# Kernel tuning notes

Hardware: AMD Instinct MI355X
Metric: run time of the kernel (lower is better)

## Reference

```python
import jax, jax.numpy as jnp
import numpy as np

N, E, H, PIN, PEIN, POUT, L = 50000, 800000, 128, 16, 8, 8, 4
EPS = 1e-7


def setup_inputs() -> dict:
    key = jax.random.key(0)
    ks = jax.random.split(key, 24)
    f = jax.random.normal
    inp = {
        'x': f(ks[0], (N, PIN), jnp.float32),
        'edge_attr': f(ks[1], (E, PEIN), jnp.float32),
        'edge_index': jax.random.randint(ks[2], (2, E), 0, N, jnp.int32),
        # encoders
        'node_W': f(ks[3], (PIN, H)) * (1.0 / np.sqrt(PIN)),
        'node_b': jnp.zeros((H,)),
        'edge_W': f(ks[4], (PEIN, H)) * (1.0 / np.sqrt(PEIN)),
        'edge_b': jnp.zeros((H,)),
        # GENConv params per layer (stacked over L): MLP Linear(H,2H)->LN->ReLU->Linear(2H,H), temp t
        'W1': f(ks[5], (L, H, 2 * H)) * (1.0 / np.sqrt(H)),
        'b1': jnp.zeros((L, 2 * H)),
        'g1': jnp.ones((L, 2 * H)),
        'be1': jnp.zeros((L, 2 * H)),
        'W2': f(ks[6], (L, 2 * H, H)) * (1.0 / np.sqrt(2 * H)),
        'b2': jnp.zeros((L, H)),
        't': jnp.ones((L,)),
        # DeepGCNLayer LayerNorms
        'ng': jnp.ones((L, H)),
        'nb': jnp.zeros((L, H)),
        # output head
        'out_W': f(ks[7], (H, POUT)) * (1.0 / np.sqrt(H)),
        'out_b': jnp.zeros((POUT,)),
    }
    return inp


def _layernorm(x, g, b):
    mu = jnp.mean(x, -1, keepdims=True)
    v = jnp.mean(jnp.square(x - mu), -1, keepdims=True)
    return (x - mu) * jax.lax.rsqrt(v + 1e-5) * g + b


def reference(x, edge_attr, edge_index, node_W, node_b, edge_W, edge_b,
              W1, b1, g1, be1, W2, b2, t, ng, nb, out_W, out_b):
    src, dst = edge_index[0], edge_index[1]

    def genconv(h, e, i):
        # message: relu(x_j + edge_attr) + eps   [E, H]
        msg = jax.nn.relu(h[src] + e) + EPS
        # softmax aggregation over edges per destination node, temperature t[i]
        s = msg * t[i]
        m = jax.ops.segment_max(s, dst, num_segments=N)  # [N, H]
        w = jnp.exp(s - m[dst])
        denom = jax.ops.segment_sum(w, dst, num_segments=N)
        agg = jax.ops.segment_sum(msg * w, dst, num_segments=N)
        agg = jnp.where(denom > 0, agg / jnp.maximum(denom, EPS), 0.0)
        # root add, then 2-layer MLP (Linear -> LN -> ReLU -> Linear)
        z = agg + h
        z = jax.nn.relu(_layernorm(z @ W1[i] + b1[i], g1[i], be1[i]))
        return z @ W2[i] + b2[i]

    h = x @ node_W + node_b                      # node encoder
    e = jax.nn.sigmoid(edge_attr @ edge_W + edge_b)  # edge encoder
    h = genconv(h, e, 0)                         # layers[0].conv only
    for i in range(1, L):                        # res+ blocks
        z = jax.nn.relu(_layernorm(h, ng[i], nb[i]))
        h = h + genconv(z, e, i)
    h = jax.nn.relu(_layernorm(h, ng[0], nb[0]))  # layers[0] norm+act; dropout=eval identity
    return h @ out_W + out_b
```

## Files before the change

kernel.cpp:

```cpp
#include <hip/hip_runtime.h>
#include <hip/hip_bf16.h>

#define NN 50000
#define NE 800000
#define HH 128
#define PIN_ 16
#define PEIN_ 8
#define POUT_ 8
#define LAYERS_ 4
#define EPSM 1e-7f

typedef __bf16 bf16x8 __attribute__((ext_vector_type(8)));
typedef float f32x4 __attribute__((ext_vector_type(4)));

union BF8 { bf16x8 v; unsigned short s[8]; };

__device__ inline unsigned short f2bf(float f) {
  unsigned int u = __float_as_uint(f);
  u += 0x7FFFu + ((u >> 16) & 1u);
  return (unsigned short)(u >> 16);
}


__global__ void count_deg_kernel(const int* __restrict__ dst, int* __restrict__ deg) {
  int i = blockIdx.x * blockDim.x + threadIdx.x;
  if (i < NE) atomicAdd(&deg[dst[i]], 1);
}

__global__ __launch_bounds__(1024) void scan_kernel(const int* __restrict__ deg,
                                                    int* __restrict__ row_ptr,
                                                    int* __restrict__ cursor, int n) {
  __shared__ int wsum[16];
  __shared__ int carry_s;
  int t = threadIdx.x;
  int lane = t & 63, wv = t >> 6;
  if (t == 0) carry_s = 0;
  __syncthreads();
  for (int base = 0; base < n; base += 1024) {
    int i = base + t;
    int v = (i < n) ? deg[i] : 0;
    int x = v;
#pragma unroll
    for (int off = 1; off < 64; off <<= 1) {
      int y = __shfl_up(x, off, 64);
      if (lane >= off) x += y;
    }
    if (lane == 63) wsum[wv] = x;
    __syncthreads();
    if (wv == 0 && lane < 16) {
      int s = wsum[lane];
#pragma unroll
      for (int off = 1; off < 16; off <<= 1) {
        int y = __shfl_up(s, off, 16);
        if (lane >= off) s += y;
      }
      wsum[lane] = s;
    }
    __syncthreads();
    int waveExcl = (wv > 0) ? wsum[wv - 1] : 0;
    int carry = carry_s;
    int excl = carry + waveExcl + x - v;
    if (i < n) { row_ptr[i] = excl; cursor[i] = excl; }
    __syncthreads();
    if (t == 1023) carry_s = carry + wsum[15];
    __syncthreads();
  }
  if (t == 0) row_ptr[n] = carry_s;
}

__global__ void scatter_kernel(const int* __restrict__ src, const int* __restrict__ dst,
                               int* __restrict__ cursor, int2* __restrict__ csr) {
  int i = blockIdx.x * blockDim.x + threadIdx.x;
  if (i < NE) {
    int d = dst[i];
    int pos = atomicAdd(&cursor[d], 1);
    csr[pos] = make_int2(src[i], i);
  }
}


__global__ __launch_bounds__(256) void prep_weights_kernel(
    const float* __restrict__ W1, const float* __restrict__ W2,
    unsigned short* __restrict__ W1T, unsigned short* __restrict__ W2T) {
  int idx = blockIdx.x * 256 + threadIdx.x;
  if (idx >= LAYERS_ * 256 * 128) return;
  int l = idx >> 15, r = idx & 32767;
  int n = r >> 7, k = r & 127;
  W1T[idx] = f2bf(W1[(l << 15) + k * 256 + n]);
  int c = r >> 8, kk = r & 255;
  W2T[idx] = f2bf(W2[(l << 15) + kk * 128 + c]);
}


__global__ __launch_bounds__(128) void node_enc_kernel(const float* __restrict__ x,
                                                       const float* __restrict__ W,
                                                       const float* __restrict__ b,
                                                       float* __restrict__ h) {
  __shared__ float xs[16 * PIN_];
  int f = threadIdx.x;
  float w[PIN_];
#pragma unroll
  for (int k = 0; k < PIN_; ++k) w[k] = W[k * HH + f];
  float bf = b[f];
  int base = blockIdx.x * 16;
  xs[f] = x[(size_t)base * PIN_ + f];
  xs[f + 128] = x[(size_t)base * PIN_ + f + 128];
  __syncthreads();
#pragma unroll
  for (int r = 0; r < 16; ++r) {
    float acc = bf;
#pragma unroll
    for (int k = 0; k < PIN_; ++k) acc = fmaf(xs[r * PIN_ + k], w[k], acc);
    h[(size_t)(base + r) * HH + f] = acc;
  }
}


__global__ __launch_bounds__(256) void aggregate_kernel(
    const int* __restrict__ row_ptr, const int2* __restrict__ csr,
    const float* __restrict__ edge_attr, const float* __restrict__ edge_W,
    const float* __restrict__ edge_b, const float* __restrict__ z,
    const float* __restrict__ t_all, int layer, float* __restrict__ u) {
  int wv = threadIdx.x >> 6, lane = threadIdx.x & 63;
  int n = blockIdx.x * 4 + wv;
  if (n >= NN) return;
  float ew0[PEIN_], ew1[PEIN_];
#pragma unroll
  for (int k = 0; k < PEIN_; ++k) {
    ew0[k] = edge_W[k * HH + lane];
    ew1[k] = edge_W[k * HH + lane + 64];
  }
  float eb0 = edge_b[lane], eb1 = edge_b[lane + 64];
  float t = t_all[layer];
  int beg = row_ptr[n], end = row_ptr[n + 1];
  float m0 = -1e30f, m1 = -1e30f, d0 = 0.f, d1 = 0.f, a0 = 0.f, a1 = 0.f;
  for (int p = beg; p < end; ++p) {
    int2 se = csr[p];
    const float4* ea = (const float4*)(edge_attr + (size_t)se.y * PEIN_);
    float4 A = ea[0], B = ea[1];
    float acc0 = eb0, acc1 = eb1;
    acc0 = fmaf(A.x, ew0[0], acc0); acc0 = fmaf(A.y, ew0[1], acc0);
    acc0 = fmaf(A.z, ew0[2], acc0); acc0 = fmaf(A.w, ew0[3], acc0);
    acc0 = fmaf(B.x, ew0[4], acc0); acc0 = fmaf(B.y, ew0[5], acc0);
    acc0 = fmaf(B.z, ew0[6], acc0); acc0 = fmaf(B.w, ew0[7], acc0);
    acc1 = fmaf(A.x, ew1[0], acc1); acc1 = fmaf(A.y, ew1[1], acc1);
    acc1 = fmaf(A.z, ew1[2], acc1); acc1 = fmaf(A.w, ew1[3], acc1);
    acc1 = fmaf(B.x, ew1[4], acc1); acc1 = fmaf(B.y, ew1[5], acc1);
    acc1 = fmaf(B.z, ew1[6], acc1); acc1 = fmaf(B.w, ew1[7], acc1);
    float e0 = __builtin_amdgcn_rcpf(1.f + __expf(-acc0));
    float e1 = __builtin_amdgcn_rcpf(1.f + __expf(-acc1));
    const float* zr = z + (size_t)se.x * HH;
    float zj0 = zr[lane], zj1 = zr[lane + 64];
    float msg0 = fmaxf(zj0 + e0, 0.f) + EPSM;
    float msg1 = fmaxf(zj1 + e1, 0.f) + EPSM;
    float s0 = msg0 * t, s1 = msg1 * t;
    float nm0 = fmaxf(m0, s0), nm1 = fmaxf(m1, s1);
    float sc0 = __expf(m0 - nm0), sc1 = __expf(m1 - nm1);
    float w0 = __expf(s0 - nm0), w1 = __expf(s1 - nm1);
    d0 = fmaf(d0, sc0, w0); d1 = fmaf(d1, sc1, w1);
    a0 = fmaf(a0, sc0, msg0 * w0); a1 = fmaf(a1, sc1, msg1 * w1);
    m0 = nm0; m1 = nm1;
  }
  float agg0 = (d0 > 0.f) ? a0 / fmaxf(d0, EPSM) : 0.f;
  float agg1 = (d1 > 0.f) ? a1 / fmaxf(d1, EPSM) : 0.f;
  const size_t ro = (size_t)n * HH;
  u[ro + lane] = agg0 + z[ro + lane];
  u[ro + lane + 64] = agg1 + z[ro + lane + 64];
}


__device__ inline int tswz(int r, int c) { return r * 256 + (c ^ ((r & 7) << 3)); }

__global__ __launch_bounds__(256) void mlp_fused_kernel(
    const float* __restrict__ uin,
    const unsigned short* __restrict__ W1T,
    const float* __restrict__ b1v, const float* __restrict__ g1v,
    const float* __restrict__ be1v,
    const unsigned short* __restrict__ W2T,
    const float* __restrict__ b2v,
    const float* __restrict__ res,
    const float* __restrict__ ngv, const float* __restrict__ nbv,
    float* __restrict__ hout, float* __restrict__ zout) {
  __shared__ __align__(16) unsigned short Tlds[4 * 16 * 256];
  int wv = threadIdx.x >> 6, lane = threadIdx.x & 63;
  int gw = blockIdx.x * 4 + wv;
  if (gw >= NN / 16) return;
  int row0 = gw * 16;
  int l15 = lane & 15, qg = lane >> 4;
  unsigned short* tl = Tlds + wv * 4096;

  BF8 afr[4];
#pragma unroll
  for (int kb = 0; kb < 4; ++kb) {
    const float* up = uin + (size_t)(row0 + l15) * HH + kb * 32 + qg * 8;
    float4 f0 = *(const float4*)up;
    float4 f1 = *(const float4*)(up + 4);
    afr[kb].s[0] = f2bf(f0.x); afr[kb].s[1] = f2bf(f0.y);
    afr[kb].s[2] = f2bf(f0.z); afr[kb].s[3] = f2bf(f0.w);
    afr[kb].s[4] = f2bf(f1.x); afr[kb].s[5] = f2bf(f1.y);
    afr[kb].s[6] = f2bf(f1.z); afr[kb].s[7] = f2bf(f1.w);
  }
  f32x4 acc1[16];
#pragma unroll
  for (int nb = 0; nb < 16; ++nb) acc1[nb] = (f32x4){0.f, 0.f, 0.f, 0.f};
#pragma unroll
  for (int nb = 0; nb < 16; ++nb) {
#pragma unroll
    for (int kb = 0; kb < 4; ++kb) {
      bf16x8 b = *(const bf16x8*)(W1T + (size_t)(nb * 16 + l15) * HH + kb * 32 + qg * 8);
      acc1[nb] = __builtin_amdgcn_mfma_f32_16x16x32_bf16(afr[kb].v, b, acc1[nb], 0, 0, 0);
    }
  }

  float sum1[4] = {0.f, 0.f, 0.f, 0.f};
#pragma unroll
  for (int nb = 0; nb < 16; ++nb) {
    float bb = b1v[nb * 16 + l15];
#pragma unroll
    for (int i = 0; i < 4; ++i) { acc1[nb][i] += bb; sum1[i] += acc1[nb][i]; }
  }
#pragma unroll
  for (int i = 0; i < 4; ++i) {
#pragma unroll
    for (int m = 1; m < 16; m <<= 1) sum1[i] += __shfl_xor(sum1[i], m, 64);
  }
  float mu1[4], sq1[4] = {0.f, 0.f, 0.f, 0.f};
#pragma unroll
  for (int i = 0; i < 4; ++i) mu1[i] = sum1[i] * (1.f / 256.f);
#pragma unroll
  for (int nb = 0; nb < 16; ++nb)
#pragma unroll
    for (int i = 0; i < 4; ++i) {
      float d = acc1[nb][i] - mu1[i];
      sq1[i] = fmaf(d, d, sq1[i]);
    }
#pragma unroll
  for (int i = 0; i < 4; ++i) {
#pragma unroll
    for (int m = 1; m < 16; m <<= 1) sq1[i] += __shfl_xor(sq1[i], m, 64);
  }
  float rstd1[4];
#pragma unroll
  for (int i = 0; i < 4; ++i) rstd1[i] = rsqrtf(sq1[i] * (1.f / 256.f) + 1e-5f);
#pragma unroll
  for (int nb = 0; nb < 16; ++nb) {
    int c = nb * 16 + l15;
    float g = g1v[c], be = be1v[c];
#pragma unroll
    for (int i = 0; i < 4; ++i) {
      float tv = fmaxf(fmaf((acc1[nb][i] - mu1[i]) * rstd1[i], g, be), 0.f);
      tl[tswz(4 * qg + i, c)] = f2bf(tv);
    }
  }

  f32x4 acc2[8];
#pragma unroll
  for (int nc = 0; nc < 8; ++nc) acc2[nc] = (f32x4){0.f, 0.f, 0.f, 0.f};
#pragma unroll
  for (int kb = 0; kb < 8; ++kb) {
    bf16x8 a2 = *(const bf16x8*)&tl[tswz(l15, kb * 32 + qg * 8)];
#pragma unroll
    for (int nc = 0; nc < 8; ++nc) {
      bf16x8 b = *(const bf16x8*)(W2T + (size_t)(nc * 16 + l15) * 256 + kb * 32 + qg * 8);
      acc2[nc] = __builtin_amdgcn_mfma_f32_16x16x32_bf16(a2, b, acc2[nc], 0, 0, 0);
    }
  }

  float sum2[4] = {0.f, 0.f, 0.f, 0.f};
#pragma unroll
  for (int nc = 0; nc < 8; ++nc) {
    int c = nc * 16 + l15;
    float bb = b2v[c];
#pragma unroll
    for (int i = 0; i < 4; ++i) {
      float v = acc2[nc][i] + bb;
      if (res) v += res[(size_t)(row0 + 4 * qg + i) * HH + c];
      acc2[nc][i] = v;
      sum2[i] += v;
    }
  }
#pragma unroll
  for (int nc = 0; nc < 8; ++nc) {
    int c = nc * 16 + l15;
#pragma unroll
    for (int i = 0; i < 4; ++i)
      hout[(size_t)(row0 + 4 * qg + i) * HH + c] = acc2[nc][i];
  }
#pragma unroll
  for (int i = 0; i < 4; ++i) {
#pragma unroll
    for (int m = 1; m < 16; m <<= 1) sum2[i] += __shfl_xor(sum2[i], m, 64);
  }
  float mu2[4], sq2[4] = {0.f, 0.f, 0.f, 0.f};
#pragma unroll
  for (int i = 0; i < 4; ++i) mu2[i] = sum2[i] * (1.f / 128.f);
#pragma unroll
  for (int nc = 0; nc < 8; ++nc)
#pragma unroll
    for (int i = 0; i < 4; ++i) {
      float d = acc2[nc][i] - mu2[i];
      sq2[i] = fmaf(d, d, sq2[i]);
    }
#pragma unroll
  for (int i = 0; i < 4; ++i) {
#pragma unroll
    for (int m = 1; m < 16; m <<= 1) sq2[i] += __shfl_xor(sq2[i], m, 64);
  }
  float rstd2[4];
#pragma unroll
  for (int i = 0; i < 4; ++i) rstd2[i] = rsqrtf(sq2[i] * (1.f / 128.f) + 1e-5f);
#pragma unroll
  for (int nc = 0; nc < 8; ++nc) {
    int c = nc * 16 + l15;
    float g = ngv[c], be = nbv[c];
#pragma unroll
    for (int i = 0; i < 4; ++i) {
      float zv = fmaxf(fmaf((acc2[nc][i] - mu2[i]) * rstd2[i], g, be), 0.f);
      zout[(size_t)(row0 + 4 * qg + i) * HH + c] = zv;
    }
  }
}


__global__ __launch_bounds__(256) void out_head_kernel(const float* __restrict__ zf,
                                                       const float* __restrict__ W,
                                                       const float* __restrict__ b,
                                                       float* __restrict__ out) {
  __shared__ float Wl[HH * POUT_];
  int t = threadIdx.x;
  for (int i = t; i < HH * POUT_; i += 256) Wl[i] = W[i];
  __syncthreads();
  int n = blockIdx.x * 32 + (t >> 3);
  int p = t & 7;
  if (n >= NN) return;
  float acc = b[p];
  const float* zr = zf + (size_t)n * HH;
#pragma unroll 8
  for (int k = 0; k < HH; ++k) acc = fmaf(zr[k], Wl[k * POUT_ + p], acc);
  out[(size_t)n * POUT_ + p] = acc;
}


extern "C" void kernel_launch(void* const* d_in, const int* in_sizes, int n_in,
                              void* d_out, int out_size, void* d_ws, size_t ws_size,
                              hipStream_t stream) {
  const float* x = (const float*)d_in[0];
  const float* edge_attr = (const float*)d_in[1];
  const int* edge_index = (const int*)d_in[2];
  const float* node_W = (const float*)d_in[3];
  const float* node_b = (const float*)d_in[4];
  const float* edge_W = (const float*)d_in[5];
  const float* edge_b = (const float*)d_in[6];
  const float* W1 = (const float*)d_in[7];
  const float* b1 = (const float*)d_in[8];
  const float* g1 = (const float*)d_in[9];
  const float* be1 = (const float*)d_in[10];
  const float* W2 = (const float*)d_in[11];
  const float* b2 = (const float*)d_in[12];
  const float* t_all = (const float*)d_in[13];
  const float* ng = (const float*)d_in[14];
  const float* nb = (const float*)d_in[15];
  const float* out_W = (const float*)d_in[16];
  const float* out_b = (const float*)d_in[17];

  const int* src = edge_index;
  const int* dst = edge_index + NE;

  char* w = (char*)d_ws;
  float* h = (float*)w;
  float* u = (float*)(w + 25600000);
  float* z = (float*)(w + 51200000);
  int* deg = (int*)(w + 76800000);
  int* row_ptr = (int*)(w + 76800000 + 204800);
  int* cursor = (int*)(w + 76800000 + 409600);
  int2* csr = (int2*)(w + 76800000 + 614400);
  unsigned short* W1Tb = (unsigned short*)(w + 83814400);
  unsigned short* W2Tb = (unsigned short*)(w + 83814400 + 262144);

  hipMemsetAsync(deg, 0, NN * sizeof(int), stream);
  count_deg_kernel<<<(NE + 255) / 256, 256, 0, stream>>>(dst, deg);
  scan_kernel<<<1, 1024, 0, stream>>>(deg, row_ptr, cursor, NN);
  scatter_kernel<<<(NE + 255) / 256, 256, 0, stream>>>(src, dst, cursor, csr);
  prep_weights_kernel<<<512, 256, 0, stream>>>(W1, W2, W1Tb, W2Tb);
  node_enc_kernel<<<NN / 16, 128, 0, stream>>>(x, node_W, node_b, h);

  const int mlp_blocks = (NN / 16 + 3) / 4;
  for (int i = 0; i < LAYERS_; ++i) {
    const float* zsrc = (i == 0) ? h : z;
    aggregate_kernel<<<NN / 4, 256, 0, stream>>>(row_ptr, csr, edge_attr, edge_W, edge_b,
                                                 zsrc, t_all, i, u);
    int zn = (i + 1) % LAYERS_;
    mlp_fused_kernel<<<mlp_blocks, 256, 0, stream>>>(
        u, W1Tb + (size_t)i * 32768, b1 + i * 256, g1 + i * 256, be1 + i * 256,
        W2Tb + (size_t)i * 32768, b2 + i * HH,
        (i == 0) ? nullptr : h,
        ng + zn * HH, nb + zn * HH, h, z);
  }
  out_head_kernel<<<(NN + 31) / 32, 256, 0, stream>>>(z, out_W, out_b, (float*)d_out);
}
```

Baseline: 1.116 ms.

## Store node features as packed bf16 and drop online max in softmax aggregation

Node activations z and aggregated u are now stored as interleaved packed bf16 pairs, which halves the bytes gathered per edge in the aggregation kernel and the bytes the MLP reads. The softmax aggregation loses its running-max rescaling and accumulates exp(msg*t) directly, removing two exps per element. This relies on msg*t staying small enough not to overflow, and it loses some precision. The MLP swaps MFMA operand order so each lane holds four consecutive columns, which allows float4 bias, gamma and output accesses and cuts the shuffle reductions to two steps. The fp32 z is written only in the last layer for the output head.

```diff
diff --git a/kernel.cpp b/kernel.cpp
--- a/kernel.cpp
+++ b/kernel.cpp
@@ -13,13 +13,16 @@
 typedef __bf16 bf16x8 __attribute__((ext_vector_type(8)));
 typedef float f32x4 __attribute__((ext_vector_type(4)));
 
-union BF8 { bf16x8 v; unsigned short s[8]; };
-
 __device__ inline unsigned short f2bf(float f) {
   unsigned int u = __float_as_uint(f);
   u += 0x7FFFu + ((u >> 16) & 1u);
   return (unsigned short)(u >> 16);
 }
+__device__ inline unsigned int packbf(float lo, float hi) {
+  return (unsigned int)f2bf(lo) | ((unsigned int)f2bf(hi) << 16);
+}
+__device__ inline float bflo(unsigned int p) { return __uint_as_float(p << 16); }
+__device__ inline float bfhi(unsigned int p) { return __uint_as_float(p & 0xFFFF0000u); }
 
 
 __global__ void count_deg_kernel(const int* __restrict__ dst, int* __restrict__ deg) {
@@ -81,37 +84,47 @@
 
 __global__ __launch_bounds__(256) void prep_weights_kernel(
     const float* __restrict__ W1, const float* __restrict__ W2,
-    unsigned short* __restrict__ W1T, unsigned short* __restrict__ W2T) {
+    unsigned short* __restrict__ W1Tp, unsigned short* __restrict__ W2T) {
   int idx = blockIdx.x * 256 + threadIdx.x;
   if (idx >= LAYERS_ * 256 * 128) return;
   int l = idx >> 15, r = idx & 32767;
-  int n = r >> 7, k = r & 127;
-  W1T[idx] = f2bf(W1[(l << 15) + k * 256 + n]);
+  int n = r >> 7, p = r & 127;
+  int k = (p >> 1) + ((p & 1) << 6);
+  W1Tp[idx] = f2bf(W1[(l << 15) + k * 256 + n]);
   int c = r >> 8, kk = r & 255;
   W2T[idx] = f2bf(W2[(l << 15) + kk * 128 + c]);
 }
 
 
-__global__ __launch_bounds__(128) void node_enc_kernel(const float* __restrict__ x,
-                                                       const float* __restrict__ W,
-                                                       const float* __restrict__ b,
-                                                       float* __restrict__ h) {
-  __shared__ float xs[16 * PIN_];
+__global__ __launch_bounds__(64) void node_enc_kernel(const float* __restrict__ x,
+                                                      const float* __restrict__ W,
+                                                      const float* __restrict__ b,
+                                                      float* __restrict__ h,
+                                                      unsigned int* __restrict__ hbp) {
+  __shared__ float xs[8 * PIN_];
   int f = threadIdx.x;
-  float w[PIN_];
-#pragma unroll
-  for (int k = 0; k < PIN_; ++k) w[k] = W[k * HH + f];
-  float bf = b[f];
-  int base = blockIdx.x * 16;
+  float w0[PIN_], w1[PIN_];
+#pragma unroll
+  for (int k = 0; k < PIN_; ++k) {
+    w0[k] = W[k * HH + f];
+    w1[k] = W[k * HH + f + 64];
+  }
+  float b0 = b[f], b1c = b[f + 64];
+  int base = blockIdx.x * 8;
   xs[f] = x[(size_t)base * PIN_ + f];
-  xs[f + 128] = x[(size_t)base * PIN_ + f + 128];
+  xs[f + 64] = x[(size_t)base * PIN_ + f + 64];
   __syncthreads();
 #pragma unroll
-  for (int r = 0; r < 16; ++r) {
-    float acc = bf;
-#pragma unroll
-    for (int k = 0; k < PIN_; ++k) acc = fmaf(xs[r * PIN_ + k], w[k], acc);
-    h[(size_t)(base + r) * HH + f] = acc;
+  for (int r = 0; r < 8; ++r) {
+    float a0 = b0, a1 = b1c;
+#pragma unroll
+    for (int k = 0; k < PIN_; ++k) {
+      a0 = fmaf(xs[r * PIN_ + k], w0[k], a0);
+      a1 = fmaf(xs[r * PIN_ + k], w1[k], a1);
+    }
+    h[(size_t)(base + r) * HH + f] = a0;
+    h[(size_t)(base + r) * HH + f + 64] = a1;
+    hbp[(size_t)(base + r) * 64 + f] = packbf(a0, a1);
   }
 }
 
@@ -119,8 +132,8 @@
 __global__ __launch_bounds__(256) void aggregate_kernel(
     const int* __restrict__ row_ptr, const int2* __restrict__ csr,
     const float* __restrict__ edge_attr, const float* __restrict__ edge_W,
-    const float* __restrict__ edge_b, const float* __restrict__ z,
-    const float* __restrict__ t_all, int layer, float* __restrict__ u) {
+    const float* __restrict__ edge_b, const unsigned int* __restrict__ zpk,
+    const float* __restrict__ t_all, int layer, unsigned int* __restrict__ upk) {
   int wv = threadIdx.x >> 6, lane = threadIdx.x & 63;
   int n = blockIdx.x * 4 + wv;
   if (n >= NN) return;
@@ -133,7 +146,8 @@
   float eb0 = edge_b[lane], eb1 = edge_b[lane + 64];
   float t = t_all[layer];
   int beg = row_ptr[n], end = row_ptr[n + 1];
-  float m0 = -1e30f, m1 = -1e30f, d0 = 0.f, d1 = 0.f, a0 = 0.f, a1 = 0.f;
+  unsigned int zs = zpk[(size_t)n * 64 + lane];
+  float d0 = 0.f, d1 = 0.f, a0 = 0.f, a1 = 0.f;
   for (int p = beg; p < end; ++p) {
     int2 se = csr[p];
     const float4* ea = (const float4*)(edge_attr + (size_t)se.y * PEIN_);
@@ -149,57 +163,47 @@
     acc1 = fmaf(B.z, ew1[6], acc1); acc1 = fmaf(B.w, ew1[7], acc1);
     float e0 = __builtin_amdgcn_rcpf(1.f + __expf(-acc0));
     float e1 = __builtin_amdgcn_rcpf(1.f + __expf(-acc1));
-    const float* zr = z + (size_t)se.x * HH;
-    float zj0 = zr[lane], zj1 = zr[lane + 64];
-    float msg0 = fmaxf(zj0 + e0, 0.f) + EPSM;
-    float msg1 = fmaxf(zj1 + e1, 0.f) + EPSM;
-    float s0 = msg0 * t, s1 = msg1 * t;
-    float nm0 = fmaxf(m0, s0), nm1 = fmaxf(m1, s1);
-    float sc0 = __expf(m0 - nm0), sc1 = __expf(m1 - nm1);
-    float w0 = __expf(s0 - nm0), w1 = __expf(s1 - nm1);
-    d0 = fmaf(d0, sc0, w0); d1 = fmaf(d1, sc1, w1);
-    a0 = fmaf(a0, sc0, msg0 * w0); a1 = fmaf(a1, sc1, msg1 * w1);
-    m0 = nm0; m1 = nm1;
+    unsigned int zp = zpk[(size_t)se.x * 64 + lane];
+    float msg0 = fmaxf(bflo(zp) + e0, 0.f) + EPSM;
+    float msg1 = fmaxf(bfhi(zp) + e1, 0.f) + EPSM;
+    float w0 = __expf(msg0 * t), w1 = __expf(msg1 * t);
+    d0 += w0; d1 += w1;
+    a0 = fmaf(msg0, w0, a0); a1 = fmaf(msg1, w1, a1);
   }
   float agg0 = (d0 > 0.f) ? a0 / fmaxf(d0, EPSM) : 0.f;
   float agg1 = (d1 > 0.f) ? a1 / fmaxf(d1, EPSM) : 0.f;
-  const size_t ro = (size_t)n * HH;
-  u[ro + lane] = agg0 + z[ro + lane];
-  u[ro + lane + 64] = agg1 + z[ro + lane + 64];
-}
-
-
-__device__ inline int tswz(int r, int c) { return r * 256 + (c ^ ((r & 7) << 3)); }
+  float u0 = agg0 + bflo(zs);
+  float u1 = agg1 + bfhi(zs);
+  upk[(size_t)n * 64 + lane] = packbf(u0, u1);
+}
+
 
 __global__ __launch_bounds__(256) void mlp_fused_kernel(
-    const float* __restrict__ uin,
-    const unsigned short* __restrict__ W1T,
+    const unsigned int* __restrict__ upk,
+    const unsigned short* __restrict__ W1Tp,
     const float* __restrict__ b1v, const float* __restrict__ g1v,
     const float* __restrict__ be1v,
     const unsigned short* __restrict__ W2T,
     const float* __restrict__ b2v,
     const float* __restrict__ res,
     const float* __restrict__ ngv, const float* __restrict__ nbv,
-    float* __restrict__ hout, float* __restrict__ zout) {
-  __shared__ __align__(16) unsigned short Tlds[4 * 16 * 256];
+    float* __restrict__ hout, float* __restrict__ zoutf,
+    unsigned int* __restrict__ zbp) {
+  __shared__ __align__(16) unsigned short Tlds[4 * 4096];
   int wv = threadIdx.x >> 6, lane = threadIdx.x & 63;
   int gw = blockIdx.x * 4 + wv;
   if (gw >= NN / 16) return;
   int row0 = gw * 16;
   int l15 = lane & 15, qg = lane >> 4;
+  int co = 4 * qg;
+  int sx = (l15 & 7) << 3;
   unsigned short* tl = Tlds + wv * 4096;
 
-  BF8 afr[4];
-#pragma unroll
-  for (int kb = 0; kb < 4; ++kb) {
-    const float* up = uin + (size_t)(row0 + l15) * HH + kb * 32 + qg * 8;
-    float4 f0 = *(const float4*)up;
-    float4 f1 = *(const float4*)(up + 4);
-    afr[kb].s[0] = f2bf(f0.x); afr[kb].s[1] = f2bf(f0.y);
-    afr[kb].s[2] = f2bf(f0.z); afr[kb].s[3] = f2bf(f0.w);
-    afr[kb].s[4] = f2bf(f1.x); afr[kb].s[5] = f2bf(f1.y);
-    afr[kb].s[6] = f2bf(f1.z); afr[kb].s[7] = f2bf(f1.w);
-  }
+  const unsigned short* ub =
+      (const unsigned short*)upk + (size_t)(row0 + l15) * HH + qg * 8;
+  bf16x8 ufr[4];
+#pragma unroll
+  for (int kb = 0; kb < 4; ++kb) ufr[kb] = *(const bf16x8*)(ub + kb * 32);
   f32x4 acc1[16];
 #pragma unroll
   for (int nb = 0; nb < 16; ++nb) acc1[nb] = (f32x4){0.f, 0.f, 0.f, 0.f};
@@ -207,117 +211,110 @@
   for (int nb = 0; nb < 16; ++nb) {
 #pragma unroll
     for (int kb = 0; kb < 4; ++kb) {
-      bf16x8 b = *(const bf16x8*)(W1T + (size_t)(nb * 16 + l15) * HH + kb * 32 + qg * 8);
-      acc1[nb] = __builtin_amdgcn_mfma_f32_16x16x32_bf16(afr[kb].v, b, acc1[nb], 0, 0, 0);
-    }
-  }
-
-  float sum1[4] = {0.f, 0.f, 0.f, 0.f};
+      bf16x8 wf = *(const bf16x8*)(W1Tp + (size_t)(nb * 16 + l15) * HH + kb * 32 + qg * 8);
+      acc1[nb] = __builtin_amdgcn_mfma_f32_16x16x32_bf16(wf, ufr[kb], acc1[nb], 0, 0, 0);
+    }
+  }
+
+  float sum1 = 0.f;
 #pragma unroll
   for (int nb = 0; nb < 16; ++nb) {
-    float bb = b1v[nb * 16 + l15];
-#pragma unroll
-    for (int i = 0; i < 4; ++i) { acc1[nb][i] += bb; sum1[i] += acc1[nb][i]; }
-  }
-#pragma unroll
-  for (int i = 0; i < 4; ++i) {
-#pragma unroll
-    for (int m = 1; m < 16; m <<= 1) sum1[i] += __shfl_xor(sum1[i], m, 64);
-  }
-  float mu1[4], sq1[4] = {0.f, 0.f, 0.f, 0.f};
-#pragma unroll
-  for (int i = 0; i < 4; ++i) mu1[i] = sum1[i] * (1.f / 256.f);
+    float4 bq = *(const float4*)(b1v + nb * 16 + co);
+    acc1[nb][0] += bq.x; acc1[nb][1] += bq.y;
+    acc1[nb][2] += bq.z; acc1[nb][3] += bq.w;
+    sum1 += acc1[nb][0] + acc1[nb][1] + acc1[nb][2] + acc1[nb][3];
+  }
+  sum1 += __shfl_xor(sum1, 16, 64);
+  sum1 += __shfl_xor(sum1, 32, 64);
+  float mu1 = sum1 * (1.f / 256.f);
+  float sq1 = 0.f;
 #pragma unroll
   for (int nb = 0; nb < 16; ++nb)
 #pragma unroll
     for (int i = 0; i < 4; ++i) {
-      float d = acc1[nb][i] - mu1[i];
-      sq1[i] = fmaf(d, d, sq1[i]);
-    }
-#pragma unroll
-  for (int i = 0; i < 4; ++i) {
-#pragma unroll
-    for (int m = 1; m < 16; m <<= 1) sq1[i] += __shfl_xor(sq1[i], m, 64);
-  }
-  float rstd1[4];
-#pragma unroll
-  for (int i = 0; i < 4; ++i) rstd1[i] = rsqrtf(sq1[i] * (1.f / 256.f) + 1e-5f);
+      float d = acc1[nb][i] - mu1;
+      sq1 = fmaf(d, d, sq1);
+    }
+  sq1 += __shfl_xor(sq1, 16, 64);
+  sq1 += __shfl_xor(sq1, 32, 64);
+  float rstd1 = rsqrtf(sq1 * (1.f / 256.f) + 1e-5f);
 #pragma unroll
   for (int nb = 0; nb < 16; ++nb) {
-    int c = nb * 16 + l15;
-    float g = g1v[c], be = be1v[c];
+    float4 gq = *(const float4*)(g1v + nb * 16 + co);
+    float4 eq = *(const float4*)(be1v + nb * 16 + co);
+    float t0 = fmaxf(fmaf((acc1[nb][0] - mu1) * rstd1, gq.x, eq.x), 0.f);
+    float t1 = fmaxf(fmaf((acc1[nb][1] - mu1) * rstd1, gq.y, eq.y), 0.f);
+    float t2 = fmaxf(fmaf((acc1[nb][2] - mu1) * rstd1, gq.z, eq.z), 0.f);
+    float t3 = fmaxf(fmaf((acc1[nb][3] - mu1) * rstd1, gq.w, eq.w), 0.f);
+    int ad = l15 * 256 + ((nb * 16 + co) ^ sx);
+    *(uint2*)(tl + ad) = make_uint2(packbf(t0, t1), packbf(t2, t3));
+  }
+
+  f32x4 acc2[8];
+#pragma unroll
+  for (int nc = 0; nc < 8; ++nc) acc2[nc] = (f32x4){0.f, 0.f, 0.f, 0.f};
+#pragma unroll
+  for (int kb = 0; kb < 8; ++kb) {
+    bf16x8 tf = *(const bf16x8*)(tl + l15 * 256 + ((kb * 32 + qg * 8) ^ sx));
+#pragma unroll
+    for (int nc = 0; nc < 8; ++nc) {
+      bf16x8 wf = *(const bf16x8*)(W2T + (size_t)(nc * 16 + l15) * 256 + kb * 32 + qg * 8);
+      acc2[nc] = __builtin_amdgcn_mfma_f32_16x16x32_bf16(wf, tf, acc2[nc], 0, 0, 0);
+    }
+  }
+
+  size_t rb = (size_t)(row0 + l15) * HH;
+  float sum2 = 0.f;
+#pragma unroll
+  for (int nc = 0; nc < 8; ++nc) {
+    float4 bq = *(const float4*)(b2v + nc * 16 + co);
+    acc2[nc][0] += bq.x; acc2[nc][1] += bq.y;
+    acc2[nc][2] += bq.z; acc2[nc][3] += bq.w;
+    if (res) {
+      float4 rq = *(const float4*)(res + rb + nc * 16 + co);
+      acc2[nc][0] += rq.x; acc2[nc][1] += rq.y;
+      acc2[nc][2] += rq.z; acc2[nc][3] += rq.w;
+    }
+    *(float4*)(hout + rb + nc * 16 + co) =
+        make_float4(acc2[nc][0], acc2[nc][1], acc2[nc][2], acc2[nc][3]);
+    sum2 += acc2[nc][0] + acc2[nc][1] + acc2[nc][2] + acc2[nc][3];
+  }
+  sum2 += __shfl_xor(sum2, 16, 64);
+  sum2 += __shfl_xor(sum2, 32, 64);
+  float mu2 = sum2 * (1.f / 128.f);
+  float sq2 = 0.f;
+#pragma unroll
+  for (int nc = 0; nc < 8; ++nc)
 #pragma unroll
     for (int i = 0; i < 4; ++i) {
-      float tv = fmaxf(fmaf((acc1[nb][i] - mu1[i]) * rstd1[i], g, be), 0.f);
-      tl[tswz(4 * qg + i, c)] = f2bf(tv);
-    }
-  }
-
-  f32x4 acc2[8];
-#pragma unroll
-  for (int nc = 0; nc < 8; ++nc) acc2[nc] = (f32x4){0.f, 0.f, 0.f, 0.f};
-#pragma unroll
-  for (int kb = 0; kb < 8; ++kb) {
-    bf16x8 a2 = *(const bf16x8*)&tl[tswz(l15, kb * 32 + qg * 8)];
-#pragma unroll
-    for (int nc = 0; nc < 8; ++nc) {
-      bf16x8 b = *(const bf16x8*)(W2T + (size_t)(nc * 16 + l15) * 256 + kb * 32 + qg * 8);
-      acc2[nc] = __builtin_amdgcn_mfma_f32_16x16x32_bf16(a2, b, acc2[nc], 0, 0, 0);
-    }
-  }
-
-  float sum2[4] = {0.f, 0.f, 0.f, 0.f};
+      float d = acc2[nc][i] - mu2;
+      sq2 = fmaf(d, d, sq2);
+    }
+  sq2 += __shfl_xor(sq2, 16, 64);
+  sq2 += __shfl_xor(sq2, 32, 64);
+  float rstd2 = rsqrtf(sq2 * (1.f / 128.f) + 1e-5f);
 #pragma unroll
   for (int nc = 0; nc < 8; ++nc) {
-    int c = nc * 16 + l15;
-    float bb = b2v[c];
-#pragma unroll
-    for (int i = 0; i < 4; ++i) {
-      float v = acc2[nc][i] + bb;
-      if (res) v += res[(size_t)(row0 + 4 * qg + i) * HH + c];
-      acc2[nc][i] = v;
-      sum2[i] += v;
-    }
-  }
-#pragma unroll
-  for (int nc = 0; nc < 8; ++nc) {
-    int c = nc * 16 + l15;
-#pragma unroll
-    for (int i = 0; i < 4; ++i)
-      hout[(size_t)(row0 + 4 * qg + i) * HH + c] = acc2[nc][i];
-  }
-#pragma unroll
-  for (int i = 0; i < 4; ++i) {
-#pragma unroll
-    for (int m = 1; m < 16; m <<= 1) sum2[i] += __shfl_xor(sum2[i], m, 64);
-  }
-  float mu2[4], sq2[4] = {0.f, 0.f, 0.f, 0.f};
-#pragma unroll
-  for (int i = 0; i < 4; ++i) mu2[i] = sum2[i] * (1.f / 128.f);
-#pragma unroll
-  for (int nc = 0; nc < 8; ++nc)
-#pragma unroll
-    for (int i = 0; i < 4; ++i) {
-      float d = acc2[nc][i] - mu2[i];
-      sq2[i] = fmaf(d, d, sq2[i]);
-    }
-#pragma unroll
-  for (int i = 0; i < 4; ++i) {
-#pragma unroll
-    for (int m = 1; m < 16; m <<= 1) sq2[i] += __shfl_xor(sq2[i], m, 64);
-  }
-  float rstd2[4];
-#pragma unroll
-  for (int i = 0; i < 4; ++i) rstd2[i] = rsqrtf(sq2[i] * (1.f / 128.f) + 1e-5f);
-#pragma unroll
-  for (int nc = 0; nc < 8; ++nc) {
-    int c = nc * 16 + l15;
-    float g = ngv[c], be = nbv[c];
-#pragma unroll
-    for (int i = 0; i < 4; ++i) {
-      float zv = fmaxf(fmaf((acc2[nc][i] - mu2[i]) * rstd2[i], g, be), 0.f);
-      zout[(size_t)(row0 + 4 * qg + i) * HH + c] = zv;
-    }
+    float4 gq = *(const float4*)(ngv + nc * 16 + co);
+    float4 eq = *(const float4*)(nbv + nc * 16 + co);
+    acc2[nc][0] = fmaxf(fmaf((acc2[nc][0] - mu2) * rstd2, gq.x, eq.x), 0.f);
+    acc2[nc][1] = fmaxf(fmaf((acc2[nc][1] - mu2) * rstd2, gq.y, eq.y), 0.f);
+    acc2[nc][2] = fmaxf(fmaf((acc2[nc][2] - mu2) * rstd2, gq.z, eq.z), 0.f);
+    acc2[nc][3] = fmaxf(fmaf((acc2[nc][3] - mu2) * rstd2, gq.w, eq.w), 0.f);
+  }
+  if (zoutf) {
+#pragma unroll
+    for (int nc = 0; nc < 8; ++nc)
+      *(float4*)(zoutf + rb + nc * 16 + co) =
+          make_float4(acc2[nc][0], acc2[nc][1], acc2[nc][2], acc2[nc][3]);
+  }
+#pragma unroll
+  for (int nc = 0; nc < 4; ++nc) {
+    *(uint4*)(zbp + (size_t)(row0 + l15) * 64 + nc * 16 + co) =
+        make_uint4(packbf(acc2[nc][0], acc2[nc + 4][0]),
+                   packbf(acc2[nc][1], acc2[nc + 4][1]),
+                   packbf(acc2[nc][2], acc2[nc + 4][2]),
+                   packbf(acc2[nc][3], acc2[nc + 4][3]));
   }
 }
 
@@ -368,33 +365,36 @@
 
   char* w = (char*)d_ws;
   float* h = (float*)w;
-  float* u = (float*)(w + 25600000);
-  float* z = (float*)(w + 51200000);
-  int* deg = (int*)(w + 76800000);
-  int* row_ptr = (int*)(w + 76800000 + 204800);
-  int* cursor = (int*)(w + 76800000 + 409600);
-  int2* csr = (int2*)(w + 76800000 + 614400);
-  unsigned short* W1Tb = (unsigned short*)(w + 83814400);
-  unsigned short* W2Tb = (unsigned short*)(w + 83814400 + 262144);
+  unsigned int* upk = (unsigned int*)(w + 25600000);
+  unsigned int* zbp = (unsigned int*)(w + 38400000);
+  unsigned int* hbp = (unsigned int*)(w + 51200000);
+  float* zf = (float*)(w + 64000000);
+  int* deg = (int*)(w + 89600000);
+  int* row_ptr = (int*)(w + 89804800);
+  int* cursor = (int*)(w + 90009600);
+  int2* csr = (int2*)(w + 90214400);
+  unsigned short* W1Tp = (unsigned short*)(w + 96614400);
+  unsigned short* W2Tb = (unsigned short*)(w + 96876544);
 
   hipMemsetAsync(deg, 0, NN * sizeof(int), stream);
   count_deg_kernel<<<(NE + 255) / 256, 256, 0, stream>>>(dst, deg);
   scan_kernel<<<1, 1024, 0, stream>>>(deg, row_ptr, cursor, NN);
   scatter_kernel<<<(NE + 255) / 256, 256, 0, stream>>>(src, dst, cursor, csr);
-  prep_weights_kernel<<<512, 256, 0, stream>>>(W1, W2, W1Tb, W2Tb);
-  node_enc_kernel<<<NN / 16, 128, 0, stream>>>(x, node_W, node_b, h);
+  prep_weights_kernel<<<512, 256, 0, stream>>>(W1, W2, W1Tp, W2Tb);
+  node_enc_kernel<<<NN / 8, 64, 0, stream>>>(x, node_W, node_b, h, hbp);
 
   const int mlp_blocks = (NN / 16 + 3) / 4;
   for (int i = 0; i < LAYERS_; ++i) {
-    const float* zsrc = (i == 0) ? h : z;
+    const unsigned int* zsrc = (i == 0) ? hbp : zbp;
     aggregate_kernel<<<NN / 4, 256, 0, stream>>>(row_ptr, csr, edge_attr, edge_W, edge_b,
-                                                 zsrc, t_all, i, u);
+                                                 zsrc, t_all, i, upk);
     int zn = (i + 1) % LAYERS_;
     mlp_fused_kernel<<<mlp_blocks, 256, 0, stream>>>(
-        u, W1Tb + (size_t)i * 32768, b1 + i * 256, g1 + i * 256, be1 + i * 256,
+        upk, W1Tp + (size_t)i * 32768, b1 + i * 256, g1 + i * 256, be1 + i * 256,
         W2Tb + (size_t)i * 32768, b2 + i * HH,
         (i == 0) ? nullptr : h,
-        ng + zn * HH, nb + zn * HH, h, z);
-  }
-  out_head_kernel<<<(NN + 31) / 32, 256, 0, stream>>>(z, out_W, out_b, (float*)d_out);
-}
+        ng + zn * HH, nb + zn * HH, h,
+        (i == LAYERS_ - 1) ? zf : nullptr, zbp);
+  }
+  out_head_kernel<<<(NN + 31) / 32, 256, 0, stream>>>(zf, out_W, out_b, (float*)d_out);
+}
```

Measured after the change: 1.039 ms. -6.9%, faster.
